# Kernel optimization log

Measured on AMD Instinct MI355X. Metric: run time of the kernel, lower is better.

The kernel has to match this reference:

```python
import jax, jax.numpy as jnp
import numpy as np

N, E, C_IN, H = 50000, 800000, 128, 128
BN_EPS = 1e-5


def gcn_conv(x, W, b, src, dst, n):
    # Dense transform then degree-normalized (GCN) neighbor aggregation with self-loops
    h = x @ W  # [N, H]
    deg = jax.ops.segment_sum(jnp.ones_like(dst, dtype=h.dtype), dst, num_segments=n)
    dinv = jax.lax.rsqrt(jnp.maximum(deg, 1.0))  # self-loops guarantee deg >= 1
    norm = dinv[src] * dinv[dst]                 # [E+N]
    msg = h[src] * norm[:, None]                 # gather + scale
    out = jax.ops.segment_sum(msg, dst, num_segments=n)  # scatter-add
    return out + b


def batchnorm(x, gamma, beta):
    mu = jnp.mean(x, axis=0)
    var = jnp.mean(jnp.square(x - mu), axis=0)  # biased var, as torch BN training
    return (x - mu) * jax.lax.rsqrt(var + BN_EPS) * gamma + beta


def setup_inputs() -> dict:
    key = jax.random.key(0)
    ks = jax.random.split(key, 8)
    node_feat = jax.random.normal(ks[0], (N, C_IN), dtype=jnp.float32)
    edge_index = jax.random.randint(ks[1], (2, E), 0, N, dtype=jnp.int64)
    s1 = 1.0 / np.sqrt(C_IN)
    s2 = 1.0 / np.sqrt(H)
    return {
        "node_feat": node_feat,
        "edge_index": edge_index,
        "W1": jax.random.uniform(ks[2], (C_IN, H), jnp.float32, -s1, s1),
        "b1": jnp.zeros((H,), jnp.float32),
        "W2": jax.random.uniform(ks[3], (H, H), jnp.float32, -s2, s2),
        "b2": jnp.zeros((H,), jnp.float32),
        "g1": jnp.ones((H,), jnp.float32),
        "beta1": jnp.zeros((H,), jnp.float32),
        "g2": jnp.ones((H,), jnp.float32),
        "beta2": jnp.zeros((H,), jnp.float32),
    }


def reference(node_feat, edge_index, W1, b1, W2, b2, g1, beta1, g2, beta2):
    n = node_feat.shape[0]
    sl = jnp.arange(n, dtype=edge_index.dtype)
    src = jnp.concatenate([edge_index[0], sl])  # add self-loops
    dst = jnp.concatenate([edge_index[1], sl])
    x = jax.nn.relu(batchnorm(gcn_conv(node_feat, W1, b1, src, dst, n), g1, beta1))
    x = jax.nn.relu(batchnorm(gcn_conv(x, W2, b2, src, dst, n), g2, beta2))
    # dropout is identity in eval / deterministic reference
    return x
```

## Files before the change

### kernel.cpp

```cpp
#include <hip/hip_runtime.h>

__device__ __forceinline__ float b2f(unsigned short u) {
    union { unsigned int i; float f; } x; x.i = ((unsigned int)u) << 16; return x.f;
}
__device__ __forceinline__ unsigned short f2b(float f) {
    union { float f; unsigned int i; } x; x.f = f;
    unsigned int r = x.i + 0x7fffu + ((x.i >> 16) & 1u);
    return (unsigned short)(r >> 16);
}
__device__ __forceinline__ bool finitef(float x) {
    union { float f; unsigned int u; } c; c.f = x;
    return ((c.u >> 23) & 0xffu) != 0xffu;
}

typedef __attribute__((ext_vector_type(8))) __bf16 bf16x8;
typedef __attribute__((ext_vector_type(4))) float f32x4;

#define HDIM 128
#define LSTR 136
#define ROWU 64
#define DCAP 62
#define NCOPY 32

__device__ __forceinline__ void bn_compute(const float* colsum, const float* colsq,
                                           const unsigned short* gam, const unsigned short* bet,
                                           int isbf, float invn, int f,
                                           float* sc_out, float* sf_out) {
    float cs = 0.f, cq = 0.f;
#pragma unroll
    for (int c = 0; c < NCOPY; ++c) {
        cs += colsum[c * 128 + f];
        cq += colsq[c * 128 + f];
    }
    float gv, bv;
    if (isbf) { gv = b2f(gam[f]);            bv = b2f(bet[f]); }
    else      { gv = ((const float*)gam)[f]; bv = ((const float*)bet)[f]; }
    if (!finitef(cs) || !finitef(cq)) { *sc_out = 0.f; *sf_out = 150.f; return; }
    float mu = cs * invn;
    float var = cq * invn - mu * mu;
    var = var < 0.f ? 0.f : var;
    float rstd = rsqrtf(var + 1e-5f);
    float s = gv * rstd;
    *sc_out = s;
    *sf_out = bv - mu * s;
}

__global__ void fill_f32(float* p, int n, float v) {
    int i = blockIdx.x * 256 + threadIdx.x;
    if (i < n) p[i] = v;
}

__global__ void prep(const unsigned short* __restrict__ X0, const int* __restrict__ ei,
                     const unsigned short* __restrict__ W1, const unsigned short* __restrict__ W2,
                     unsigned short* __restrict__ Wt1, unsigned short* __restrict__ Wt2,
                     int* __restrict__ zbase, int zcount, int* __restrict__ flags) {
    int bid = blockIdx.x, tid = threadIdx.x;
    if (bid < 128) {
        __shared__ int sane, hi64;
        if (tid == 0) { sane = 0; hi64 = 0; }
        __syncthreads();
        unsigned short u = X0[2 * tid];
        int e = (u >> 7) & 0xff;
        if (e >= 100 && e <= 140) atomicAdd(&sane, 1);
        if (bid == 0 && tid < 64) {
            if (ei[2 * tid + 1] != 0) atomicAdd(&hi64, 1);
        }
        __syncthreads();
        int isbf = (sane >= 128) ? 1 : 0;
        if (bid == 0 && tid == 0) { flags[0] = isbf; flags[1] = (hi64 == 0) ? 1 : 0; }
        int idx = bid * 256 + tid;
        const unsigned short* src; unsigned short* dst; int l;
        if (idx < 16384) { src = W1; dst = Wt1; l = idx; }
        else             { src = W2; dst = Wt2; l = idx - 16384; }
        int k = l >> 7, c = l & 127;
        unsigned short v = isbf ? src[l] : f2b(((const float*)src)[l]);
        dst[c * 128 + k] = v;
    } else {
        int i = (bid - 128) * 256 + tid;
        if (i < zcount) zbase[i] = 0;
    }
}

__global__ void scatter1(const int* __restrict__ ei, unsigned short* __restrict__ csr2d,
                         const int* __restrict__ flags, int E, int N) {
    int is64 = flags[1];
    int e = blockIdx.x * 256 + threadIdx.x;
    if (e < E) {
        int s, d;
        if (is64) { s = ei[2 * (size_t)e]; d = ei[2 * (size_t)E + 2 * (size_t)e]; }
        else      { s = ei[e];             d = ei[(size_t)E + e]; }
        s = s < 0 ? 0 : (s >= N ? N - 1 : s);
        d = d < 0 ? 0 : (d >= N ? N - 1 : d);
        unsigned short* row = &csr2d[(size_t)d * ROWU];
        int slot = atomicAdd((int*)row, 1);
        if (slot < DCAP) row[2 + slot] = (unsigned short)s;
    }
}

__global__ __launch_bounds__(256) void gemm_mfma(
    const unsigned short* __restrict__ A, const unsigned short* __restrict__ Wt,
    unsigned short* __restrict__ C, const int* __restrict__ aflag, int mode,
    const float* __restrict__ colsum, const float* __restrict__ colsq,
    const unsigned short* __restrict__ gam, const unsigned short* __restrict__ bet,
    float invn, const unsigned short* __restrict__ csr2d, int n) {
    __shared__ __align__(16) unsigned short Wl[128 * LSTR];
    __shared__ __align__(16) unsigned short Al[64 * LSTR];
    __shared__ float sc_sh[128], sf_sh[128];
    int tid = threadIdx.x;
    int row0 = blockIdx.x * 64;
    int isbf = aflag[0];

    if (mode == 2 && tid < 128)
        bn_compute(colsum, colsq, gam, bet, isbf, invn, tid, &sc_sh[tid], &sf_sh[tid]);

    const uint4* Wg = (const uint4*)Wt;
#pragma unroll
    for (int it = 0; it < 8; ++it) {
        int idx = tid + it * 256;
        int nn = idx >> 4, k8 = idx & 15;
        *(uint4*)&Wl[nn * LSTR + k8 * 8] = Wg[idx];
    }
    if (mode == 2) __syncthreads();

    int amode = (mode == 2) ? 2 : isbf;
    if (amode == 1) {
        const uint4* Ag = (const uint4*)A;
        for (int it = 0; it < 4; ++it) {
            int idx = tid + it * 256;
            int r = idx >> 4, cc = idx & 15;
            int gr = row0 + r;
            uint4 v; v.x = v.y = v.z = v.w = 0u;
            if (gr < n) v = Ag[(size_t)gr * 16 + cc];
            *(uint4*)&Al[r * LSTR + cc * 8] = v;
        }
    } else if (amode == 0) {
        const uint4* Af = (const uint4*)A;
        for (int it = 0; it < 8; ++it) {
            int idx = tid + it * 256;
            int r = idx >> 5, c4 = idx & 31;
            int gr = row0 + r;
            uint4 v; v.x = v.y = v.z = v.w = 0u;
            if (gr < n) v = Af[(size_t)gr * 32 + c4];
            float ff[4]; *(uint4*)ff = v;
            ushort4 o;
            o.x = f2b(ff[0]); o.y = f2b(ff[1]); o.z = f2b(ff[2]); o.w = f2b(ff[3]);
            *(ushort4*)&Al[r * LSTR + c4 * 4] = o;
        }
    } else {
        const uint4* Ag = (const uint4*)A;
        for (int it = 0; it < 4; ++it) {
            int idx = tid + it * 256;
            int r = idx >> 4, cc = idx & 15;
            int gr = row0 + r;
            uint4 v; v.x = v.y = v.z = v.w = 0u;
            if (gr < n) v = Ag[(size_t)gr * 16 + cc];
            unsigned short hu[8]; *(uint4*)hu = v;
            unsigned short ou[8];
#pragma unroll
            for (int j = 0; j < 8; ++j) {
                int f = cc * 8 + j;
                float x = b2f(hu[j]) * sc_sh[f] + sf_sh[f];
                ou[j] = f2b(x > 0.f ? x : 0.f);
            }
            *(uint4*)&Al[r * LSTR + cc * 8] = *(uint4*)ou;
        }
    }
    __syncthreads();

    int wave = tid >> 6, lane = tid & 63;
    int m = lane & 15, quad = lane >> 4;

    bf16x8 afr[4];
#pragma unroll
    for (int kc = 0; kc < 4; ++kc)
        afr[kc] = *(const bf16x8*)&Al[(wave * 16 + m) * LSTR + kc * 32 + quad * 8];

    float dv[4];
#pragma unroll
    for (int i2 = 0; i2 < 4; ++i2) {
        int gr = row0 + wave * 16 + quad * 4 + i2;
        if (gr < n) {
            int ct = *(const int*)&csr2d[(size_t)gr * ROWU];
            dv[i2] = rsqrtf((float)ct + 1.0f);
        } else dv[i2] = 0.f;
    }

    for (int t = 0; t < 8; ++t) {
        f32x4 acc = {0.f, 0.f, 0.f, 0.f};
#pragma unroll
        for (int kc = 0; kc < 4; ++kc) {
            bf16x8 bfr = *(const bf16x8*)&Wl[(t * 16 + m) * LSTR + kc * 32 + quad * 8];
            acc = __builtin_amdgcn_mfma_f32_16x16x32_bf16(afr[kc], bfr, acc, 0, 0, 0);
        }
#pragma unroll
        for (int i2 = 0; i2 < 4; ++i2) {
            int gr = row0 + wave * 16 + quad * 4 + i2;
            if (gr < n) C[(size_t)gr * 128 + t * 16 + m] = f2b(acc[i2] * dv[i2]);
        }
    }
}

__global__ __launch_bounds__(256) void agg_stats(
    const unsigned short* __restrict__ Hb, const unsigned short* __restrict__ csr2d,
    unsigned short* __restrict__ AGG,
    float* __restrict__ colsum, float* __restrict__ colsq, int n) {
    int tid = threadIdx.x;
    int wave = tid >> 6, lane = tid & 63;
    int g = lane >> 4, q = lane & 15;

    float s1[8], s2[8];
#pragma unroll
    for (int j = 0; j < 8; ++j) { s1[j] = 0.f; s2[j] = 0.f; }

    for (int i = blockIdx.x * 4 + wave; i < n; i += gridDim.x * 4) {
        const unsigned short* row = &csr2d[(size_t)i * ROWU];
        int ct = *(const int*)row;
        float di = rsqrtf((float)ct + 1.0f);
        int c = ct < DCAP ? ct : DCAP;
        const unsigned short* adj = row + 2;
        float acc[8];
#pragma unroll
        for (int j = 0; j < 8; ++j) acc[j] = 0.f;

        if (g == 0) {
            uint4 a4 = *(const uint4*)&Hb[(size_t)i * 128 + q * 8];
            unsigned short au[8]; *(uint4*)au = a4;
#pragma unroll
            for (int j = 0; j < 8; ++j) acc[j] += b2f(au[j]);
        }

        int t = g;
        for (; t + 12 < c; t += 16) {
            int sA = adj[t];
            int sB = adj[t + 4];
            int sC = adj[t + 8];
            int sD = adj[t + 12];
            uint4 a4 = *(const uint4*)&Hb[(size_t)sA * 128 + q * 8];
            uint4 b4 = *(const uint4*)&Hb[(size_t)sB * 128 + q * 8];
            uint4 c4 = *(const uint4*)&Hb[(size_t)sC * 128 + q * 8];
            uint4 d4 = *(const uint4*)&Hb[(size_t)sD * 128 + q * 8];
            unsigned short au[8]; *(uint4*)au = a4;
            unsigned short bu[8]; *(uint4*)bu = b4;
            unsigned short cu[8]; *(uint4*)cu = c4;
            unsigned short du[8]; *(uint4*)du = d4;
#pragma unroll
            for (int j = 0; j < 8; ++j)
                acc[j] += (b2f(au[j]) + b2f(bu[j])) + (b2f(cu[j]) + b2f(du[j]));
        }
        for (; t < c; t += 4) {
            int sA = adj[t];
            uint4 a4 = *(const uint4*)&Hb[(size_t)sA * 128 + q * 8];
            unsigned short au[8]; *(uint4*)au = a4;
#pragma unroll
            for (int j = 0; j < 8; ++j) acc[j] += b2f(au[j]);
        }

#pragma unroll
        for (int j = 0; j < 8; ++j) {
            acc[j] += __shfl_xor(acc[j], 16, 64);
            acc[j] += __shfl_xor(acc[j], 32, 64);
            acc[j] *= di;
        }
        if (g == 0) {
            unsigned short ou[8];
#pragma unroll
            for (int j = 0; j < 8; ++j) {
                float v = acc[j];
                ou[j] = f2b(v);
                s1[j] += v; s2[j] += v * v;
            }
            *(uint4*)&AGG[(size_t)i * 128 + q * 8] = *(uint4*)ou;
        }
    }

    __shared__ float sh[4][256];
    if (g == 0) {
#pragma unroll
        for (int j = 0; j < 8; ++j) {
            sh[wave][q * 8 + j] = s1[j];
            sh[wave][128 + q * 8 + j] = s2[j];
        }
    }
    __syncthreads();
    if (tid < 128) {
        float a = sh[0][tid] + sh[1][tid] + sh[2][tid] + sh[3][tid];
        float b = sh[0][128 + tid] + sh[1][128 + tid] + sh[2][128 + tid] + sh[3][128 + tid];
        int copy = blockIdx.x & (NCOPY - 1);
        atomicAdd(&colsum[copy * 128 + tid], a);
        atomicAdd(&colsq[copy * 128 + tid], b);
    }
}

__global__ void bn_apply_f32(const unsigned short* __restrict__ AGG,
                             const float* __restrict__ colsum, const float* __restrict__ colsq,
                             const unsigned short* __restrict__ gam, const unsigned short* __restrict__ bet,
                             const int* __restrict__ flag, float invn,
                             float* __restrict__ out, int nchunk) {
    __shared__ float sc_sh[128], sf_sh[128];
    int tid = threadIdx.x;
    if (tid < 128)
        bn_compute(colsum, colsq, gam, bet, flag[0], invn, tid, &sc_sh[tid], &sf_sh[tid]);
    __syncthreads();
    int i = blockIdx.x * 256 + tid;
    if (i >= nchunk) return;
    int base = i * 8;
    int f0 = base & 127;
    uint4 hv = *(const uint4*)&AGG[base];
    unsigned short hu[8]; *(uint4*)hu = hv;
    float o[8];
#pragma unroll
    for (int j = 0; j < 8; ++j) {
        float v = b2f(hu[j]) * sc_sh[f0 + j] + sf_sh[f0 + j];
        o[j] = v > 0.f ? v : 0.f;
    }
    *(float4*)&out[base] = *(float4*)&o[0];
    *(float4*)&out[base + 4] = *(float4*)&o[4];
}

extern "C" void kernel_launch(void* const* d_in, const int* in_sizes, int n_in,
                              void* d_out, int out_size, void* d_ws, size_t ws_size,
                              hipStream_t stream) {
    const unsigned short* X0 = (const unsigned short*)d_in[0];
    const int* ei = (const int*)d_in[1];
    const unsigned short* W1 = (const unsigned short*)d_in[2];
    const unsigned short* W2 = (const unsigned short*)d_in[4];
    const unsigned short* g1 = (const unsigned short*)d_in[6];
    const unsigned short* be1 = (const unsigned short*)d_in[7];
    const unsigned short* g2 = (const unsigned short*)d_in[8];
    const unsigned short* be2 = (const unsigned short*)d_in[9];
    float* OUT = (float*)d_out;

    int N = in_sizes[0] / HDIM;
    int E = in_sizes[1] / 2;
    int total = N * HDIM;
    int applyb = (total + 255) / 256;

    bool ok = (n_in == 10) && (N > 0) && (in_sizes[0] == N * HDIM) && (E > 0)
           && (in_sizes[2] == HDIM * HDIM) && (in_sizes[4] == HDIM * HDIM)
           && (in_sizes[6] == HDIM) && (in_sizes[9] == HDIM) && (out_size == total)
           && (N <= 65536);
    if (!ok) { fill_f32<<<applyb, 256, 0, stream>>>(OUT, total, -100.0f); return; }

    size_t need = 256 + (size_t)N * ROWU * 2 + (size_t)NCOPY * 512 * 4 + 16 + 256
                + (size_t)total * 4 + 65536 + 1024;
    if (ws_size < need) { fill_f32<<<applyb, 256, 0, stream>>>(OUT, total, -300.0f); return; }

    char* w = (char*)d_ws;
    w = (char*)(((uintptr_t)w + 255) & ~(uintptr_t)255);
    unsigned short* csr2d = (unsigned short*)w; w += (size_t)N * ROWU * 2;
    float* stats = (float*)w; w += (size_t)NCOPY * 512 * 4;
    int* flags = (int*)w;     w += 16;
    w = (char*)(((uintptr_t)w + 255) & ~(uintptr_t)255);
    unsigned short* Hb = (unsigned short*)w;  w += (size_t)total * 2;
    unsigned short* AGG = (unsigned short*)w; w += (size_t)total * 2;
    unsigned short* Wt1 = (unsigned short*)w; w += (size_t)HDIM * HDIM * 2;
    unsigned short* Wt2 = (unsigned short*)w; w += (size_t)HDIM * HDIM * 2;

    float* colsum1 = stats;
    float* colsq1 = stats + NCOPY * 128;
    float* colsum2 = stats + 2 * NCOPY * 128;
    float* colsq2 = stats + 3 * NCOPY * 128;

    int ebl = (E + 255) / 256;
    int gemmb = (N + 63) / 64;
    float invn = 1.0f / (float)N;
    int zcount = N * (ROWU / 2) + NCOPY * 512;

    prep<<<128 + (zcount + 255) / 256, 256, 0, stream>>>(X0, ei, W1, W2, Wt1, Wt2,
                                                         (int*)csr2d, zcount, flags);
    scatter1<<<ebl, 256, 0, stream>>>(ei, csr2d, flags, E, N);

    gemm_mfma<<<gemmb, 256, 0, stream>>>(X0, Wt1, Hb, flags, -1,
                                         nullptr, nullptr, nullptr, nullptr, invn, csr2d, N);
    agg_stats<<<2048, 256, 0, stream>>>(Hb, csr2d, AGG, colsum1, colsq1, N);

    gemm_mfma<<<gemmb, 256, 0, stream>>>(AGG, Wt2, Hb, flags, 2,
                                         colsum1, colsq1, g1, be1, invn, csr2d, N);
    agg_stats<<<2048, 256, 0, stream>>>(Hb, csr2d, AGG, colsum2, colsq2, N);

    bn_apply_f32<<<(total / 8 + 255) / 256, 256, 0, stream>>>(AGG, colsum2, colsq2,
                                                              g2, be2, flags, invn, OUT, total / 8);
}
```

Baseline: 256.1 us.

## Split features into XCD-local column slabs for aggregation locality

The Hb and AGG intermediates move from row-major [N,128] to four column slabs of [N,32]. Each aggregation block is mapped by its XCD id to one slab, so each XCD's L2 only has to cache a quarter of the gathered feature matrix. Each node is now handled by 4 lanes instead of a full wave, with per-lane neighbor loops, nontemporal loads and stores for CSR and output, and a shuffle-based stats reduction. The GEMM and bn_apply are changed to write and read the slab layout. The approach relies on blocks being dispatched round-robin across XCDs, and it shortens the per-lane memory parallelism for each node.

After: 274.8 us. 1.07x slower.

```diff
diff --git a/kernel.cpp b/kernel.cpp
--- a/kernel.cpp
+++ b/kernel.cpp
@@ -15,12 +15,15 @@
 
 typedef __attribute__((ext_vector_type(8))) __bf16 bf16x8;
 typedef __attribute__((ext_vector_type(4))) float f32x4;
+typedef __attribute__((ext_vector_type(4))) unsigned int u32x4;
 
 #define HDIM 128
 #define LSTR 136
 #define ROWU 64
 #define DCAP 62
 #define NCOPY 32
+#define AGG_BLOCKS 2048
+#define AGG_GROUPS 32768
 
 __device__ __forceinline__ void bn_compute(const float* colsum, const float* colsq,
                                            const unsigned short* gam, const unsigned short* bet,
@@ -109,6 +112,7 @@
     int tid = threadIdx.x;
     int row0 = blockIdx.x * 64;
     int isbf = aflag[0];
+    size_t cs = (size_t)n * 32;
 
     if (mode == 2 && tid < 128)
         bn_compute(colsum, colsq, gam, bet, isbf, invn, tid, &sc_sh[tid], &sf_sh[tid]);
@@ -148,12 +152,13 @@
         }
     } else {
         const uint4* Ag = (const uint4*)A;
+        size_t cs4 = (size_t)n * 4;
         for (int it = 0; it < 4; ++it) {
             int idx = tid + it * 256;
             int r = idx >> 4, cc = idx & 15;
             int gr = row0 + r;
             uint4 v; v.x = v.y = v.z = v.w = 0u;
-            if (gr < n) v = Ag[(size_t)gr * 16 + cc];
+            if (gr < n) v = Ag[(size_t)(cc >> 2) * cs4 + (size_t)gr * 4 + (cc & 3)];
             unsigned short hu[8]; *(uint4*)hu = v;
             unsigned short ou[8];
 #pragma unroll
@@ -192,10 +197,11 @@
             bf16x8 bfr = *(const bf16x8*)&Wl[(t * 16 + m) * LSTR + kc * 32 + quad * 8];
             acc = __builtin_amdgcn_mfma_f32_16x16x32_bf16(afr[kc], bfr, acc, 0, 0, 0);
         }
+        size_t tb = (size_t)(t >> 1) * cs + (size_t)((t & 1) * 16 + m);
 #pragma unroll
         for (int i2 = 0; i2 < 4; ++i2) {
             int gr = row0 + wave * 16 + quad * 4 + i2;
-            if (gr < n) C[(size_t)gr * 128 + t * 16 + m] = f2b(acc[i2] * dv[i2]);
+            if (gr < n) C[tb + (size_t)gr * 32] = f2b(acc[i2] * dv[i2]);
         }
     }
 }
@@ -205,89 +211,90 @@
     unsigned short* __restrict__ AGG,
     float* __restrict__ colsum, float* __restrict__ colsq, int n) {
     int tid = threadIdx.x;
+    int bid = blockIdx.x;
     int wave = tid >> 6, lane = tid & 63;
-    int g = lane >> 4, q = lane & 15;
+    int ns = lane >> 2, lq = lane & 3;
+    int xcd = bid & 7;
+    int fc = xcd >> 1;
+    size_t cbase = (size_t)fc * (size_t)n * 32;
+    int wid = (((bid >> 3) << 1) | (xcd & 1)) * 4 + wave;
+    int gid = wid * 16 + ns;
 
     float s1[8], s2[8];
 #pragma unroll
     for (int j = 0; j < 8; ++j) { s1[j] = 0.f; s2[j] = 0.f; }
 
-    for (int i = blockIdx.x * 4 + wave; i < n; i += gridDim.x * 4) {
-        const unsigned short* row = &csr2d[(size_t)i * ROWU];
-        int ct = *(const int*)row;
+    for (int nd = gid; nd < n; nd += AGG_GROUPS) {
+        const unsigned short* row = &csr2d[(size_t)nd * ROWU];
+        int ct = __builtin_nontemporal_load((const int*)row);
         float di = rsqrtf((float)ct + 1.0f);
         int c = ct < DCAP ? ct : DCAP;
         const unsigned short* adj = row + 2;
+
         float acc[8];
-#pragma unroll
-        for (int j = 0; j < 8; ++j) acc[j] = 0.f;
-
-        if (g == 0) {
-            uint4 a4 = *(const uint4*)&Hb[(size_t)i * 128 + q * 8];
-            unsigned short au[8]; *(uint4*)au = a4;
-#pragma unroll
-            for (int j = 0; j < 8; ++j) acc[j] += b2f(au[j]);
-        }
-
-        int t = g;
-        for (; t + 12 < c; t += 16) {
-            int sA = adj[t];
-            int sB = adj[t + 4];
-            int sC = adj[t + 8];
-            int sD = adj[t + 12];
-            uint4 a4 = *(const uint4*)&Hb[(size_t)sA * 128 + q * 8];
-            uint4 b4 = *(const uint4*)&Hb[(size_t)sB * 128 + q * 8];
-            uint4 c4 = *(const uint4*)&Hb[(size_t)sC * 128 + q * 8];
-            uint4 d4 = *(const uint4*)&Hb[(size_t)sD * 128 + q * 8];
-            unsigned short au[8]; *(uint4*)au = a4;
-            unsigned short bu[8]; *(uint4*)bu = b4;
-            unsigned short cu[8]; *(uint4*)cu = c4;
-            unsigned short du[8]; *(uint4*)du = d4;
+        u32x4 v0 = *(const u32x4*)&Hb[cbase + (size_t)nd * 32 + lq * 8];
+        unsigned short su[8]; *(u32x4*)su = v0;
+#pragma unroll
+        for (int j = 0; j < 8; ++j) acc[j] = b2f(su[j]);
+
+        int t = 0;
+        for (; t + 3 < c; t += 4) {
+            int sA = (int)__builtin_nontemporal_load(&adj[t]);
+            int sB = (int)__builtin_nontemporal_load(&adj[t + 1]);
+            int sC = (int)__builtin_nontemporal_load(&adj[t + 2]);
+            int sD = (int)__builtin_nontemporal_load(&adj[t + 3]);
+            u32x4 a4 = *(const u32x4*)&Hb[cbase + (size_t)sA * 32 + lq * 8];
+            u32x4 b4 = *(const u32x4*)&Hb[cbase + (size_t)sB * 32 + lq * 8];
+            u32x4 c4 = *(const u32x4*)&Hb[cbase + (size_t)sC * 32 + lq * 8];
+            u32x4 d4 = *(const u32x4*)&Hb[cbase + (size_t)sD * 32 + lq * 8];
+            unsigned short au[8]; *(u32x4*)au = a4;
+            unsigned short bu[8]; *(u32x4*)bu = b4;
+            unsigned short cu[8]; *(u32x4*)cu = c4;
+            unsigned short du[8]; *(u32x4*)du = d4;
 #pragma unroll
             for (int j = 0; j < 8; ++j)
                 acc[j] += (b2f(au[j]) + b2f(bu[j])) + (b2f(cu[j]) + b2f(du[j]));
         }
-        for (; t < c; t += 4) {
-            int sA = adj[t];
-            uint4 a4 = *(const uint4*)&Hb[(size_t)sA * 128 + q * 8];
-            unsigned short au[8]; *(uint4*)au = a4;
+        for (; t < c; ++t) {
+            int sA = (int)__builtin_nontemporal_load(&adj[t]);
+            u32x4 a4 = *(const u32x4*)&Hb[cbase + (size_t)sA * 32 + lq * 8];
+            unsigned short au[8]; *(u32x4*)au = a4;
 #pragma unroll
             for (int j = 0; j < 8; ++j) acc[j] += b2f(au[j]);
         }
 
+        unsigned short ou[8];
 #pragma unroll
         for (int j = 0; j < 8; ++j) {
-            acc[j] += __shfl_xor(acc[j], 16, 64);
-            acc[j] += __shfl_xor(acc[j], 32, 64);
-            acc[j] *= di;
-        }
-        if (g == 0) {
-            unsigned short ou[8];
-#pragma unroll
-            for (int j = 0; j < 8; ++j) {
-                float v = acc[j];
-                ou[j] = f2b(v);
-                s1[j] += v; s2[j] += v * v;
-            }
-            *(uint4*)&AGG[(size_t)i * 128 + q * 8] = *(uint4*)ou;
-        }
-    }
-
-    __shared__ float sh[4][256];
-    if (g == 0) {
+            float v = acc[j] * di;
+            ou[j] = f2b(v);
+            s1[j] += v; s2[j] += v * v;
+        }
+        __builtin_nontemporal_store(*(u32x4*)ou, (u32x4*)&AGG[cbase + (size_t)nd * 32 + lq * 8]);
+    }
+
+#pragma unroll
+    for (int off = 4; off <= 32; off <<= 1) {
 #pragma unroll
         for (int j = 0; j < 8; ++j) {
-            sh[wave][q * 8 + j] = s1[j];
-            sh[wave][128 + q * 8 + j] = s2[j];
+            s1[j] += __shfl_xor(s1[j], off, 64);
+            s2[j] += __shfl_xor(s2[j], off, 64);
+        }
+    }
+    __shared__ float sh[4][64];
+    if (lane < 4) {
+#pragma unroll
+        for (int j = 0; j < 8; ++j) {
+            sh[wave][lq * 8 + j] = s1[j];
+            sh[wave][32 + lq * 8 + j] = s2[j];
         }
     }
     __syncthreads();
-    if (tid < 128) {
+    if (tid < 64) {
         float a = sh[0][tid] + sh[1][tid] + sh[2][tid] + sh[3][tid];
-        float b = sh[0][128 + tid] + sh[1][128 + tid] + sh[2][128 + tid] + sh[3][128 + tid];
-        int copy = blockIdx.x & (NCOPY - 1);
-        atomicAdd(&colsum[copy * 128 + tid], a);
-        atomicAdd(&colsq[copy * 128 + tid], b);
+        int copy = bid & (NCOPY - 1);
+        if (tid < 32) atomicAdd(&colsum[copy * 128 + fc * 32 + tid], a);
+        else          atomicAdd(&colsq[copy * 128 + fc * 32 + (tid & 31)], a);
     }
 }
 
@@ -295,7 +302,7 @@
                              const float* __restrict__ colsum, const float* __restrict__ colsq,
                              const unsigned short* __restrict__ gam, const unsigned short* __restrict__ bet,
                              const int* __restrict__ flag, float invn,
-                             float* __restrict__ out, int nchunk) {
+                             float* __restrict__ out, int nchunk, int n) {
     __shared__ float sc_sh[128], sf_sh[128];
     int tid = threadIdx.x;
     if (tid < 128)
@@ -304,8 +311,10 @@
     int i = blockIdx.x * 256 + tid;
     if (i >= nchunk) return;
     int base = i * 8;
+    int node = base >> 7;
     int f0 = base & 127;
-    uint4 hv = *(const uint4*)&AGG[base];
+    size_t cs = (size_t)n * 32;
+    uint4 hv = *(const uint4*)&AGG[(size_t)(f0 >> 5) * cs + (size_t)node * 32 + (f0 & 31)];
     unsigned short hu[8]; *(uint4*)hu = hv;
     float o[8];
 #pragma unroll
@@ -372,12 +381,12 @@
 
     gemm_mfma<<<gemmb, 256, 0, stream>>>(X0, Wt1, Hb, flags, -1,
                                          nullptr, nullptr, nullptr, nullptr, invn, csr2d, N);
-    agg_stats<<<2048, 256, 0, stream>>>(Hb, csr2d, AGG, colsum1, colsq1, N);
+    agg_stats<<<AGG_BLOCKS, 256, 0, stream>>>(Hb, csr2d, AGG, colsum1, colsq1, N);
 
     gemm_mfma<<<gemmb, 256, 0, stream>>>(AGG, Wt2, Hb, flags, 2,
                                          colsum1, colsq1, g1, be1, invn, csr2d, N);
-    agg_stats<<<2048, 256, 0, stream>>>(Hb, csr2d, AGG, colsum2, colsq2, N);
+    agg_stats<<<AGG_BLOCKS, 256, 0, stream>>>(Hb, csr2d, AGG, colsum2, colsq2, N);
 
     bn_apply_f32<<<(total / 8 + 255) / 256, 256, 0, stream>>>(AGG, colsum2, colsq2,
-                                                              g2, be2, flags, invn, OUT, total / 8);
-}
+                                                              g2, be2, flags, invn, OUT, total / 8, N);
+}
```

## Build padded CSR via two-pass destination binning with shared-memory rows

Applied to the files above, without the earlier changes.

Replaces the global-atomic per-edge scatter into the padded adjacency table with two passes. The first bins edges by destination range into 256 buckets using block-local shared counters. The second builds each bucket's rows in LDS and writes them out with coalesced stores. This removes the need to zero the whole table up front and avoids scattered global atomics. In exchange it adds an extra kernel launch and a bucket buffer, and edges beyond BCAP per bucket or rows beyond 256 nodes per bucket (N>65536) would be dropped.

Result: faster. 239.2 us, median of 4 (-6.6%).

```diff
diff --git a/kernel.cpp b/kernel.cpp
--- a/kernel.cpp
+++ b/kernel.cpp
@@ -21,6 +21,8 @@
 #define ROWU 64
 #define DCAP 62
 #define NCOPY 32
+#define NB 256
+#define BCAP 8192
 
 __device__ __forceinline__ void bn_compute(const float* colsum, const float* colsq,
                                            const unsigned short* gam, const unsigned short* bet,
@@ -81,20 +83,76 @@
     }
 }
 
-__global__ void scatter1(const int* __restrict__ ei, unsigned short* __restrict__ csr2d,
-                         const int* __restrict__ flags, int E, int N) {
+__global__ __launch_bounds__(256) void bin_edges(const int* __restrict__ ei,
+                                                 unsigned int* __restrict__ bData,
+                                                 unsigned int* __restrict__ bCnt,
+                                                 const int* __restrict__ flags,
+                                                 int E, int N, int BSZ) {
+    __shared__ unsigned int cnt[NB];
+    __shared__ unsigned int base[NB];
+    int tid = threadIdx.x;
     int is64 = flags[1];
-    int e = blockIdx.x * 256 + threadIdx.x;
-    if (e < E) {
-        int s, d;
-        if (is64) { s = ei[2 * (size_t)e]; d = ei[2 * (size_t)E + 2 * (size_t)e]; }
-        else      { s = ei[e];             d = ei[(size_t)E + e]; }
-        s = s < 0 ? 0 : (s >= N ? N - 1 : s);
-        d = d < 0 ? 0 : (d >= N ? N - 1 : d);
-        unsigned short* row = &csr2d[(size_t)d * ROWU];
-        int slot = atomicAdd((int*)row, 1);
-        if (slot < DCAP) row[2 + slot] = (unsigned short)s;
-    }
+    int e0 = blockIdx.x * 4096;
+    cnt[tid] = 0;
+    __syncthreads();
+    unsigned int val[16], loff[16]; int bk[16];
+#pragma unroll
+    for (int j = 0; j < 16; ++j) {
+        int e = e0 + j * 256 + tid;
+        bk[j] = -1;
+        if (e < E) {
+            int d, s;
+            if (is64) { d = ei[2 * (size_t)E + 2 * (size_t)e]; s = ei[2 * (size_t)e]; }
+            else      { d = ei[(size_t)E + e];                 s = ei[e]; }
+            d = d < 0 ? 0 : (d >= N ? N - 1 : d);
+            s = s < 0 ? 0 : (s >= N ? N - 1 : s);
+            int b = d / BSZ;
+            int loc = d - b * BSZ;
+            val[j] = (unsigned int)s | ((unsigned int)loc << 16);
+            bk[j] = b;
+            loff[j] = atomicAdd(&cnt[b], 1u);
+        }
+    }
+    __syncthreads();
+    unsigned int c = cnt[tid];
+    base[tid] = (c > 0) ? atomicAdd(&bCnt[tid], c) : 0u;
+    __syncthreads();
+#pragma unroll
+    for (int j = 0; j < 16; ++j) {
+        if (bk[j] >= 0) {
+            unsigned int pos = base[bk[j]] + loff[j];
+            if (pos < BCAP) bData[(size_t)bk[j] * BCAP + pos] = val[j];
+        }
+    }
+}
+
+__global__ __launch_bounds__(256) void build_csr(const unsigned int* __restrict__ bData,
+                                                 const unsigned int* __restrict__ bCnt,
+                                                 unsigned short* __restrict__ csr2d,
+                                                 int N, int BSZ) {
+    __shared__ __align__(16) unsigned short rows[256 * ROWU];
+    int b = blockIdx.x;
+    int tid = threadIdx.x;
+    int node0 = b * BSZ;
+    int nn = N - node0; if (nn > BSZ) nn = BSZ;
+    if (nn <= 0) return;
+    uint4* r4 = (uint4*)rows;
+#pragma unroll
+    for (int i = 0; i < 8; ++i) { uint4 z = {0u, 0u, 0u, 0u}; r4[tid + i * 256] = z; }
+    __syncthreads();
+    unsigned int ne = bCnt[b]; if (ne > BCAP) ne = BCAP;
+    const unsigned int* bd = &bData[(size_t)b * BCAP];
+    for (unsigned int t = tid; t < ne; t += 256) {
+        unsigned int v = bd[t];
+        unsigned int loc = v >> 16;
+        unsigned int s = v & 0xffffu;
+        unsigned int c = atomicAdd((unsigned int*)&rows[loc * ROWU], 1u);
+        if (c < DCAP) rows[loc * ROWU + 2 + c] = (unsigned short)s;
+    }
+    __syncthreads();
+    uint4* g4 = (uint4*)&csr2d[(size_t)node0 * ROWU];
+    int tot = nn * (ROWU / 8);
+    for (int i = tid; i < tot; i += 256) g4[i] = r4[i];
 }
 
 __global__ __launch_bounds__(256) void gemm_mfma(
@@ -341,34 +399,38 @@
            && (N <= 65536);
     if (!ok) { fill_f32<<<applyb, 256, 0, stream>>>(OUT, total, -100.0f); return; }
 
-    size_t need = 256 + (size_t)N * ROWU * 2 + (size_t)NCOPY * 512 * 4 + 16 + 256
-                + (size_t)total * 4 + 65536 + 1024;
+    size_t need = 1024 + (size_t)N * ROWU * 2 + (size_t)NCOPY * 512 * 4 + NB * 4 + 64
+                + (size_t)total * 4 + 65536 + (size_t)NB * BCAP * 4 + 4096;
     if (ws_size < need) { fill_f32<<<applyb, 256, 0, stream>>>(OUT, total, -300.0f); return; }
 
     char* w = (char*)d_ws;
     w = (char*)(((uintptr_t)w + 255) & ~(uintptr_t)255);
     unsigned short* csr2d = (unsigned short*)w; w += (size_t)N * ROWU * 2;
     float* stats = (float*)w; w += (size_t)NCOPY * 512 * 4;
-    int* flags = (int*)w;     w += 16;
+    unsigned int* bCnt = (unsigned int*)w; w += NB * 4;
+    int* flags = (int*)w;     w += 64;
     w = (char*)(((uintptr_t)w + 255) & ~(uintptr_t)255);
     unsigned short* Hb = (unsigned short*)w;  w += (size_t)total * 2;
     unsigned short* AGG = (unsigned short*)w; w += (size_t)total * 2;
     unsigned short* Wt1 = (unsigned short*)w; w += (size_t)HDIM * HDIM * 2;
     unsigned short* Wt2 = (unsigned short*)w; w += (size_t)HDIM * HDIM * 2;
+    w = (char*)(((uintptr_t)w + 255) & ~(uintptr_t)255);
+    unsigned int* bData = (unsigned int*)w; w += (size_t)NB * BCAP * 4;
 
     float* colsum1 = stats;
     float* colsq1 = stats + NCOPY * 128;
     float* colsum2 = stats + 2 * NCOPY * 128;
     float* colsq2 = stats + 3 * NCOPY * 128;
 
-    int ebl = (E + 255) / 256;
     int gemmb = (N + 63) / 64;
     float invn = 1.0f / (float)N;
-    int zcount = N * (ROWU / 2) + NCOPY * 512;
+    int BSZ = (N + NB - 1) / NB;
+    int zcount = NCOPY * 512 + NB;
 
     prep<<<128 + (zcount + 255) / 256, 256, 0, stream>>>(X0, ei, W1, W2, Wt1, Wt2,
-                                                         (int*)csr2d, zcount, flags);
-    scatter1<<<ebl, 256, 0, stream>>>(ei, csr2d, flags, E, N);
+                                                         (int*)stats, zcount, flags);
+    bin_edges<<<(E + 4095) / 4096, 256, 0, stream>>>(ei, bData, bCnt, flags, E, N, BSZ);
+    build_csr<<<NB, 256, 0, stream>>>(bData, bCnt, csr2d, N, BSZ);
 
     gemm_mfma<<<gemmb, 256, 0, stream>>>(X0, Wt1, Hb, flags, -1,
                                          nullptr, nullptr, nullptr, nullptr, invn, csr2d, N);
```
